# Optimization experiments

Hardware: AMD Instinct MI355X
Metric: run time of the kernel (lower is better)

Reference implementation:

```python
import jax, jax.numpy as jnp
import numpy as np

# ---- module constants (from init_kwargs) ----
NOF_LINKS = 64
NOISE = 1e-3          # gen_para.input_noise_power
DT = 0.01             # gen_para.dt
T_END = 5.12          # t
TXP = 1.0             # gen_para.tx_power
LAM = 1.0
RHO = 1.0

T_ARR = jnp.arange(0.0, T_END, DT, dtype=jnp.float32)   # [T] time grid
POW2T = jnp.power(jnp.float32(2.0), T_ARR)               # 2^t
POW2T_1 = POW2T - 1.0                                    # 2^t - 1
LN2 = jnp.log(jnp.float32(2.0))


def setup_inputs() -> dict:
    key = jax.random.key(0)
    k1, k2 = jax.random.split(key)
    pathloss = jax.random.uniform(k1, (NOF_LINKS, NOF_LINKS), dtype=jnp.float32)
    powers = jax.random.uniform(k2, (16, 20, NOF_LINKS), dtype=jnp.float32)
    return {"pathloss": pathloss, "powers": powers}


def _outage(pathloss, power):
    # power: [B, N, L]; pathloss: [L, L]
    B, N, L = power.shape
    T = T_ARR.shape[0]
    # signal[b,n,i,j] = pathloss[i,j] * power[b,n,i]  (per original expand/permute)
    y_ii = jnp.diagonal(pathloss)[None, None, :] * power              # [B,N,L]
    y_tot = power * jnp.sum(pathloss, axis=1)[None, None, :]          # sum_j signal
    y_ij = y_tot - y_ii
    sinr = y_ii / (y_ij + NOISE)                                      # [B,N,L]

    # block-0 outage CDF over time grid: Q1[b,i,t] = 1 - exp(-(2^t-1) * sinr[b,0,i])
    Q1 = 1.0 - jnp.exp(-POW2T_1[None, None, :] * sinr[:, 0, :, None])  # [B,L,T]

    # per-block pdf kernels for n >= 1 (vectorized over all blocks up front)
    s = sinr[:, 1:, :, None]                                          # [B,N-1,L,1]
    q = jnp.exp(-POW2T_1 * s) * POW2T * s * LN2                       # [B,N-1,L,T]

    def step(Q, qn):
        # Q, qn: [B,L,T]; per-channel grouped cross-correlation (torch conv1d semantics)
        x = Q.reshape(1, B * L, T)
        w = qn.reshape(B * L, 1, T)
        out = jax.lax.conv_general_dilated(
            x, w, window_strides=(1,), padding=[(T - 1, T - 1)],
            feature_group_count=B * L)                                 # [1,B*L,2T-1]
        Qn = out[0, :, :T].reshape(B, L, T) * DT
        return Qn, Qn[:, :, -1]

    q_scan = jnp.moveaxis(q, 1, 0)                                    # [N-1,B,L,T]
    _, outa_rest = jax.lax.scan(step, Q1, q_scan)                     # [N-1,B,L]
    outa = jnp.concatenate([Q1[None, :, :, -1], outa_rest], axis=0)   # [N,B,L]
    return jnp.moveaxis(outa, 0, 1)                                   # [B,N,L]


def reference(pathloss, powers):
    power = powers * TXP
    N = power.shape[1]
    outa = _outage(pathloss, power)                                   # [B,N,L]
    E = power[:, 0, :] + jnp.sum(power[:, 1:, :] * outa[:, :N - 1, :], axis=1)
    D = 1.0 + jnp.sum(outa[:, :N - 1, :], axis=1)
    loss = jnp.sum(E) + LAM * jnp.sum(outa[:, N - 1, :]) + RHO * jnp.sum(D)
    return loss
```

## Files before the change

### kernel.cpp

```cpp
#include <hip/hip_runtime.h>

#define LL 64
#define NN 20
#define DTC 0.01f
#define NOISEC 1e-3f
#define LN2C 0.69314718056f

typedef __attribute__((ext_vector_type(8))) short short8x;
typedef __attribute__((ext_vector_type(4))) float f32x4;

__device__ __forceinline__ unsigned bf16r(float x) {
    union { float f; unsigned u; } a; a.f = x;
    return (a.u + (0x7fffu + ((a.u >> 16) & 1u))) >> 16;
}
__device__ __forceinline__ unsigned pk_bf16(float x, float y) {
    return bf16r(x) | (bf16r(y) << 16);
}

__global__ __launch_bounds__(64, 1) void outage_kernel(
    const float* __restrict__ pathloss,
    const float* __restrict__ powers,
    float* __restrict__ out)
{
    __shared__ __align__(16) unsigned short gt[2][8][544];
    __shared__ __align__(16) unsigned short Qb[2][1024];

    const int lane = threadIdx.x;
    const int c = blockIdx.x, b = c >> 6, l = c & 63;
    const int nh = lane & 15;
    const int qd = lane >> 4;

    const float pl = pathloss[l * LL + lane];
    float rs = pl;
    #pragma unroll
    for (int mk = 1; mk < 64; mk <<= 1) rs += __shfl_xor(rs, mk, 64);
    const float dg   = __shfl(pl, l, 64);
    const float dsum = rs - dg;

    float P2[8], P1[8];
    #pragma unroll
    for (int u = 0; u < 8; ++u) {
        P2[u] = exp2f((8 * lane + u) * DTC);
        P1[u] = P2[u] - 1.f;
    }

    *((uint4*)&Qb[0][0] + lane) = uint4{0u, 0u, 0u, 0u};
    *((uint4*)&Qb[1][0] + lane) = uint4{0u, 0u, 0u, 0u};
    {
        const int bb = lane >> 5, w = lane & 31;
        #pragma unroll
        for (int k = 0; k < 8; ++k) gt[bb][k][512 + w] = 0;
    }

    const float p0 = powers[(b * NN + 0) * LL + l];
    const float s0 = dg * p0 / (p0 * dsum + NOISEC);
    float q7;
    {
        float v[8];
        #pragma unroll
        for (int u = 0; u < 8; ++u) v[u] = 1.f - expf(-P1[u] * s0);
        q7 = v[7];
        uint4 d4 = { pk_bf16(v[0], v[1]), pk_bf16(v[2], v[3]),
                     pk_bf16(v[4], v[5]), pk_bf16(v[6], v[7]) };
        *(uint4*)&Qb[0][512 + 8 * lane] = d4;
    }

    const float p1v = powers[(b * NN + 1) * LL + l];
    float lossCh = 1.f + p0 + (p1v + 1.f) * q7;

    auto fill_g = [&](int buf, float p) {
        float s  = dg * p / (p * dsum + NOISEC);
        float cm = s * LN2C * DTC;
        unsigned F[8];
        #pragma unroll
        for (int w = 0; w < 4; ++w) {
            float a  = expf(-P1[2 * w] * s) * P2[2 * w] * cm;
            float bb = expf(-P1[2 * w + 1] * s) * P2[2 * w + 1] * cm;
            F[w] = pk_bf16(a, bb);
        }
        #pragma unroll
        for (int w = 0; w < 4; ++w) {
            unsigned t = (unsigned)__shfl_down((int)F[w], 1, 64);
            F[4 + w] = (lane == 63) ? 0u : t;
        }
        unsigned E[7];
        #pragma unroll
        for (int j = 0; j < 7; ++j) E[j] = (F[j] >> 16) | (F[j + 1] << 16);
        #pragma unroll
        for (int k = 0; k < 8; ++k) {
            uint4 d4;
            if ((k & 1) == 0) d4 = uint4{F[k / 2], F[k / 2 + 1], F[k / 2 + 2], F[k / 2 + 3]};
            else              d4 = uint4{E[k / 2], E[k / 2 + 1], E[k / 2 + 2], E[k / 2 + 3]};
            *(uint4*)&gt[buf][k][8 * lane] = d4;
        }
    };
    fill_g(1, p1v);

    const int kk    = (7 - nh) & 7;
    const int baseA = 511 - nh + 8 * qd - kk;
    const int baseB = 512 + 32 * nh + 8 * qd;
    const int dstw  = 512 + 32 * nh + 4 * qd;

    float pnext = powers[(b * NN + 2) * LL + l];

    for (int n = 1; n < NN; ++n) {
        const unsigned short* psrc = &Qb[(n + 1) & 1][0];
        const unsigned short* pg   = &gt[n & 1][kk][0];
        unsigned short* pdst       = &Qb[n & 1][0];

        float pfut = 0.f;
        if (n <= NN - 3) pfut = powers[(b * NN + n + 2) * LL + l];

        short8x Bv[16], A0v[16], A1v[16];
        #pragma unroll
        for (int d = 0; d < 16; ++d) {
            Bv[d]  = *(const short8x*)&psrc[baseB - 32 * d];
            A0v[d] = *(const short8x*)&pg[baseA - 32 * d];
            A1v[d] = *(const short8x*)&pg[baseA - 32 * d - 16];
        }

        if (n < NN - 1) fill_g((n + 1) & 1, pnext);

        f32x4 acc0a = {0.f, 0.f, 0.f, 0.f}, acc0b = {0.f, 0.f, 0.f, 0.f};
        f32x4 acc1a = {0.f, 0.f, 0.f, 0.f}, acc1b = {0.f, 0.f, 0.f, 0.f};
        #pragma unroll
        for (int d = 0; d < 16; d += 2) {
            acc0a = __builtin_amdgcn_mfma_f32_16x16x32_bf16(A0v[d],     Bv[d],     acc0a, 0, 0, 0);
            acc1a = __builtin_amdgcn_mfma_f32_16x16x32_bf16(A1v[d],     Bv[d],     acc1a, 0, 0, 0);
            acc0b = __builtin_amdgcn_mfma_f32_16x16x32_bf16(A0v[d + 1], Bv[d + 1], acc0b, 0, 0, 0);
            acc1b = __builtin_amdgcn_mfma_f32_16x16x32_bf16(A1v[d + 1], Bv[d + 1], acc1b, 0, 0, 0);
        }
        f32x4 acc0 = acc0a + acc0b;
        f32x4 acc1 = acc1a + acc1b;

        *(uint2*)&pdst[dstw]      = uint2{pk_bf16(acc0.x, acc0.y), pk_bf16(acc0.z, acc0.w)};
        *(uint2*)&pdst[dstw + 16] = uint2{pk_bf16(acc1.x, acc1.y), pk_bf16(acc1.z, acc1.w)};

        float wgt = (n < NN - 1) ? (pnext + 1.f) : 1.f;
        lossCh += wgt * acc1.w;
        pnext = pfut;
    }

    if (lane == 63) atomicAdd(out, lossCh);
}

extern "C" void kernel_launch(void* const* d_in, const int* in_sizes, int n_in,
                              void* d_out, int out_size, void* d_ws, size_t ws_size,
                              hipStream_t stream) {
    const float* pathloss = (const float*)d_in[0];
    const float* powers   = (const float*)d_in[1];
    float* outp = (float*)d_out;

    (void)hipMemsetAsync(d_out, 0, sizeof(float) * out_size, stream);
    outage_kernel<<<16 * LL, 64, 0, stream>>>(pathloss, powers, outp);
}
```

Measured before the change: 89.80 us.

## Split per-channel convolution reduction across two waves with LDS partial-sum exchange

Each block now runs two wavefronts instead of one. Each wave handles half of the 16 MFMA reduction steps of the Toeplitz cross-correlation and half of the g-table fill. The waves swap partial accumulators through shared memory so each wave finishes one output half. The aim is to shorten the serial per-step chain and raise MFMA/ALU parallelism, at the cost of two block barriers per time step plus extra LDS traffic.

```diff
diff --git a/kernel.cpp b/kernel.cpp
--- a/kernel.cpp
+++ b/kernel.cpp
@@ -17,15 +17,18 @@
     return bf16r(x) | (bf16r(y) << 16);
 }
 
-__global__ __launch_bounds__(64, 1) void outage_kernel(
+__global__ __launch_bounds__(128, 2) void outage_kernel(
     const float* __restrict__ pathloss,
     const float* __restrict__ powers,
     float* __restrict__ out)
 {
     __shared__ __align__(16) unsigned short gt[2][8][544];
     __shared__ __align__(16) unsigned short Qb[2][1024];
+    __shared__ __align__(16) float pc[2][64][4];
 
-    const int lane = threadIdx.x;
+    const int tid  = threadIdx.x;
+    const int wv   = tid >> 6;
+    const int lane = tid & 63;
     const int c = blockIdx.x, b = c >> 6, l = c & 63;
     const int nh = lane & 15;
     const int qd = lane >> 4;
@@ -44,29 +47,29 @@
         P1[u] = P2[u] - 1.f;
     }
 
-    *((uint4*)&Qb[0][0] + lane) = uint4{0u, 0u, 0u, 0u};
-    *((uint4*)&Qb[1][0] + lane) = uint4{0u, 0u, 0u, 0u};
+    if (tid < 64) *((uint4*)&Qb[0][0] + tid)        = uint4{0u, 0u, 0u, 0u};
+    else          *((uint4*)&Qb[1][0] + (tid - 64)) = uint4{0u, 0u, 0u, 0u};
     {
-        const int bb = lane >> 5, w = lane & 31;
-        #pragma unroll
-        for (int k = 0; k < 8; ++k) gt[bb][k][512 + w] = 0;
+        const int buf = tid >> 6, k = (tid >> 3) & 7, w = tid & 7;
+        *(uint2*)&gt[buf][k][512 + 4 * w] = uint2{0u, 0u};
     }
 
     const float p0 = powers[(b * NN + 0) * LL + l];
     const float s0 = dg * p0 / (p0 * dsum + NOISEC);
-    float q7;
+    float q7 = 0.f;
     {
-        float v[8];
+        float v[4];
         #pragma unroll
-        for (int u = 0; u < 8; ++u) v[u] = 1.f - expf(-P1[u] * s0);
-        q7 = v[7];
-        uint4 d4 = { pk_bf16(v[0], v[1]), pk_bf16(v[2], v[3]),
-                     pk_bf16(v[4], v[5]), pk_bf16(v[6], v[7]) };
-        *(uint4*)&Qb[0][512 + 8 * lane] = d4;
+        for (int u = 0; u < 4; ++u) {
+            float t2 = exp2f((4 * tid + u) * DTC);
+            v[u] = 1.f - expf(-(t2 - 1.f) * s0);
+        }
+        q7 = v[3];
+        *(uint2*)&Qb[0][512 + 4 * tid] = uint2{pk_bf16(v[0], v[1]), pk_bf16(v[2], v[3])};
     }
 
     const float p1v = powers[(b * NN + 1) * LL + l];
-    float lossCh = 1.f + p0 + (p1v + 1.f) * q7;
+    float lossCh = (tid == 127) ? (1.f + p0 + (p1v + 1.f) * q7) : 0.f;
 
     auto fill_g = [&](int buf, float p) {
         float s  = dg * p / (p * dsum + NOISEC);
@@ -86,20 +89,25 @@
         unsigned E[7];
         #pragma unroll
         for (int j = 0; j < 7; ++j) E[j] = (F[j] >> 16) | (F[j + 1] << 16);
-        #pragma unroll
-        for (int k = 0; k < 8; ++k) {
-            uint4 d4;
-            if ((k & 1) == 0) d4 = uint4{F[k / 2], F[k / 2 + 1], F[k / 2 + 2], F[k / 2 + 3]};
-            else              d4 = uint4{E[k / 2], E[k / 2 + 1], E[k / 2 + 2], E[k / 2 + 3]};
-            *(uint4*)&gt[buf][k][8 * lane] = d4;
+        if (wv == 0) {
+            *(uint4*)&gt[buf][0][8 * lane] = uint4{F[0], F[1], F[2], F[3]};
+            *(uint4*)&gt[buf][1][8 * lane] = uint4{E[0], E[1], E[2], E[3]};
+            *(uint4*)&gt[buf][2][8 * lane] = uint4{F[1], F[2], F[3], F[4]};
+            *(uint4*)&gt[buf][3][8 * lane] = uint4{E[1], E[2], E[3], E[4]};
+        } else {
+            *(uint4*)&gt[buf][4][8 * lane] = uint4{F[2], F[3], F[4], F[5]};
+            *(uint4*)&gt[buf][5][8 * lane] = uint4{E[2], E[3], E[4], E[5]};
+            *(uint4*)&gt[buf][6][8 * lane] = uint4{F[3], F[4], F[5], F[6]};
+            *(uint4*)&gt[buf][7][8 * lane] = uint4{E[3], E[4], E[5], E[6]};
         }
     };
     fill_g(1, p1v);
+    __syncthreads();
 
     const int kk    = (7 - nh) & 7;
-    const int baseA = 511 - nh + 8 * qd - kk;
-    const int baseB = 512 + 32 * nh + 8 * qd;
-    const int dstw  = 512 + 32 * nh + 4 * qd;
+    const int baseA = 511 - nh + 8 * qd - kk - 256 * wv;
+    const int baseB = 512 + 32 * nh + 8 * qd - 256 * wv;
+    const int dstw  = 512 + 32 * nh + 4 * qd + 16 * wv;
 
     float pnext = powers[(b * NN + 2) * LL + l];
 
@@ -108,40 +116,49 @@
         const unsigned short* pg   = &gt[n & 1][kk][0];
         unsigned short* pdst       = &Qb[n & 1][0];
 
-        float pfut = 0.f;
-        if (n <= NN - 3) pfut = powers[(b * NN + n + 2) * LL + l];
-
-        short8x Bv[16], A0v[16], A1v[16];
+        short8x Bv[8], A0v[8], A1v[8];
         #pragma unroll
-        for (int d = 0; d < 16; ++d) {
-            Bv[d]  = *(const short8x*)&psrc[baseB - 32 * d];
+        for (int d = 0; d < 8; ++d) Bv[d] = *(const short8x*)&psrc[baseB - 32 * d];
+        #pragma unroll
+        for (int d = 0; d < 8; ++d) {
             A0v[d] = *(const short8x*)&pg[baseA - 32 * d];
             A1v[d] = *(const short8x*)&pg[baseA - 32 * d - 16];
         }
 
-        if (n < NN - 1) fill_g((n + 1) & 1, pnext);
+        float pfut = 0.f;
+        if (n < NN - 1) {
+            if (n <= NN - 3) pfut = powers[(b * NN + n + 2) * LL + l];
+            fill_g((n + 1) & 1, pnext);
+        }
 
-        f32x4 acc0a = {0.f, 0.f, 0.f, 0.f}, acc0b = {0.f, 0.f, 0.f, 0.f};
-        f32x4 acc1a = {0.f, 0.f, 0.f, 0.f}, acc1b = {0.f, 0.f, 0.f, 0.f};
+        f32x4 a0a = {0.f,0.f,0.f,0.f}, a0b = {0.f,0.f,0.f,0.f};
+        f32x4 a1a = {0.f,0.f,0.f,0.f}, a1b = {0.f,0.f,0.f,0.f};
         #pragma unroll
-        for (int d = 0; d < 16; d += 2) {
-            acc0a = __builtin_amdgcn_mfma_f32_16x16x32_bf16(A0v[d],     Bv[d],     acc0a, 0, 0, 0);
-            acc1a = __builtin_amdgcn_mfma_f32_16x16x32_bf16(A1v[d],     Bv[d],     acc1a, 0, 0, 0);
-            acc0b = __builtin_amdgcn_mfma_f32_16x16x32_bf16(A0v[d + 1], Bv[d + 1], acc0b, 0, 0, 0);
-            acc1b = __builtin_amdgcn_mfma_f32_16x16x32_bf16(A1v[d + 1], Bv[d + 1], acc1b, 0, 0, 0);
+        for (int d = 0; d < 8; d += 2) {
+            a0a = __builtin_amdgcn_mfma_f32_16x16x32_bf16(A0v[d],     Bv[d],     a0a, 0, 0, 0);
+            a1a = __builtin_amdgcn_mfma_f32_16x16x32_bf16(A1v[d],     Bv[d],     a1a, 0, 0, 0);
+            a0b = __builtin_amdgcn_mfma_f32_16x16x32_bf16(A0v[d + 1], Bv[d + 1], a0b, 0, 0, 0);
+            a1b = __builtin_amdgcn_mfma_f32_16x16x32_bf16(A1v[d + 1], Bv[d + 1], a1b, 0, 0, 0);
         }
-        f32x4 acc0 = acc0a + acc0b;
-        f32x4 acc1 = acc1a + acc1b;
+        f32x4 acc0 = a0a + a0b;
+        f32x4 acc1 = a1a + a1b;
 
-        *(uint2*)&pdst[dstw]      = uint2{pk_bf16(acc0.x, acc0.y), pk_bf16(acc0.z, acc0.w)};
-        *(uint2*)&pdst[dstw + 16] = uint2{pk_bf16(acc1.x, acc1.y), pk_bf16(acc1.z, acc1.w)};
+        f32x4 ship = wv ? acc0 : acc1;
+        f32x4 keep = wv ? acc1 : acc0;
+        *(f32x4*)&pc[wv][lane][0] = ship;
+        __syncthreads();
+
+        f32x4 tot = keep + *(const f32x4*)&pc[1 - wv][lane][0];
+
+        *(uint2*)&pdst[dstw] = uint2{pk_bf16(tot.x, tot.y), pk_bf16(tot.z, tot.w)};
 
         float wgt = (n < NN - 1) ? (pnext + 1.f) : 1.f;
-        lossCh += wgt * acc1.w;
+        if (tid == 127) lossCh += wgt * tot.w;
         pnext = pfut;
+        __syncthreads();
     }
 
-    if (lane == 63) atomicAdd(out, lossCh);
+    if (tid == 127) atomicAdd(out, lossCh);
 }
 
 extern "C" void kernel_launch(void* const* d_in, const int* in_sizes, int n_in,
@@ -152,5 +169,5 @@
     float* outp = (float*)d_out;
 
     (void)hipMemsetAsync(d_out, 0, sizeof(float) * out_size, stream);
-    outage_kernel<<<16 * LL, 64, 0, stream>>>(pathloss, powers, outp);
+    outage_kernel<<<16 * LL, 128, 0, stream>>>(pathloss, powers, outp);
 }
```

Result: slower. 93.99 us (+4.7%).
